# Kernel optimization log

Measured on AMD Instinct MI355X. Metric: run time of the kernel, lower is better.

The kernel has to match this reference:

```python
import jax, jax.numpy as jnp
import numpy as np

DIM = 1024
D_STATE = 16

def setup_inputs() -> dict:
    key = jax.random.key(0)
    kx, ka, kd = jax.random.split(key, 3)
    x = jax.random.normal(kx, (4, 8192, DIM), dtype=jnp.float32)
    A = jax.random.normal(ka, (DIM, D_STATE), dtype=jnp.float32)
    D = jax.random.normal(kd, (D_STATE, DIM), dtype=jnp.float32)
    return {"x": x, "A": A, "D": D}

def reference(x, A, D):
    # x: [B, N, C]; A: [C, S]; D: [S, C]
    x_state = jnp.einsum('bnc,cs->bns', x, A)        # [B, N, S]
    x_state = jnp.cumsum(x_state, axis=1)            # prefix sum over sequence
    out = jnp.einsum('bns,sc->bnc', x_state, D)      # [B, N, C]
    return out
```

## Files before the change

### kernel.cpp

```cpp
#include <hip/hip_runtime.h>

#define DIM   1024
#define DST   16
#define NSEQ  8192
#define NB    4

#define MT    64
#define KC    128
#define KCP   132
#define NTILE 128

__global__ __launch_bounds__(256) void kA_gemm_scan(
    const float* __restrict__ x, const float* __restrict__ A,
    float* __restrict__ Tloc, float* __restrict__ TS)
{
    __shared__ float xs[MT * KC];
    __shared__ float at[DST * KCP];
    __shared__ float scanbuf[16 * DST];

    const int t    = threadIdx.x;
    const int b    = blockIdx.x >> 7;
    const int tile = blockIdx.x & 127;
    const int n0   = tile * MT;

    const int kq4 = t >> 6;
    const int mg  = (t >> 2) & 15;
    const int sp  = t & 3;

    const float* xrow = x + ((long)(b * NSEQ + n0)) * DIM;

    float acc[4][4];
    #pragma unroll
    for (int r = 0; r < 4; ++r)
        #pragma unroll
        for (int j = 0; j < 4; ++j) acc[r][j] = 0.f;

    const int kbase = kq4 * 32;

    for (int kc = 0; kc < DIM; kc += KC) {
        {
            const int q  = t & 31;
            const int r0 = t >> 5;
            #pragma unroll
            for (int it = 0; it < 8; ++it) {
                const int m  = it * 8 + r0;
                const float4 v = *(const float4*)(xrow + (long)m * DIM + kc + 4 * q);
                const int qs = q ^ ((m >> 2) & 7);
                *(float4*)&xs[m * KC + 4 * qs] = v;
            }
        }
        {
            #pragma unroll
            for (int it = 0; it < 8; ++it) {
                const int idx = it * 256 + t;
                const int kl  = idx >> 4;
                const int ss  = idx & 15;
                at[ss * KCP + kl] = A[(kc + kl) * DST + ss];
            }
        }
        __syncthreads();

        #pragma unroll
        for (int kq = 0; kq < 8; ++kq) {
            const int kqi = (kbase >> 2) + kq;
            const float4 a0 = *(const float4*)&at[(sp +  0) * KCP + kbase + 4 * kq];
            const float4 a1 = *(const float4*)&at[(sp +  4) * KCP + kbase + 4 * kq];
            const float4 a2 = *(const float4*)&at[(sp +  8) * KCP + kbase + 4 * kq];
            const float4 a3 = *(const float4*)&at[(sp + 12) * KCP + kbase + 4 * kq];
            const int qs = kqi ^ (mg & 7);
            #pragma unroll
            for (int r = 0; r < 4; ++r) {
                const float4 xv = *(const float4*)&xs[(mg * 4 + r) * KC + 4 * qs];
                acc[r][0] += xv.x * a0.x + xv.y * a0.y + xv.z * a0.z + xv.w * a0.w;
                acc[r][1] += xv.x * a1.x + xv.y * a1.y + xv.z * a1.z + xv.w * a1.w;
                acc[r][2] += xv.x * a2.x + xv.y * a2.y + xv.z * a2.z + xv.w * a2.w;
                acc[r][3] += xv.x * a3.x + xv.y * a3.y + xv.z * a3.z + xv.w * a3.w;
            }
        }
        __syncthreads();
    }

    float* red = xs;
    #pragma unroll
    for (int r = 0; r < 4; ++r)
        #pragma unroll
        for (int j = 0; j < 4; ++j)
            red[kq4 * (64 * 17) + (mg * 4 + r) * 17 + (sp + 4 * j)] = acc[r][j];
    __syncthreads();

    const int s   = t & 15;
    const int mg2 = t >> 4;
    float acc0 = 0.f, acc1 = 0.f, acc2 = 0.f, acc3 = 0.f;
    #pragma unroll
    for (int q = 0; q < 4; ++q) {
        const float* rq = red + q * (64 * 17) + (mg2 * 4) * 17 + s;
        acc0 += rq[0 * 17];
        acc1 += rq[1 * 17];
        acc2 += rq[2 * 17];
        acc3 += rq[3 * 17];
    }
    __syncthreads();

    const float rsum = acc0 + acc1 + acc2 + acc3;
    scanbuf[mg2 * DST + s] = rsum;
    __syncthreads();
    float excl = 0.f, total = 0.f;
    #pragma unroll
    for (int m = 0; m < 16; ++m) {
        const float v = scanbuf[m * DST + s];
        total += v;
        excl  += (m < mg2) ? v : 0.f;
    }
    if (mg2 == 0) TS[((long)b * NTILE + tile) * DST + s] = total;

    const float c0 = excl + acc0;
    const float c1 = c0 + acc1;
    const float c2 = c1 + acc2;
    const float c3 = c2 + acc3;
    *(float4*)&Tloc[((long)(b * DST + s)) * NSEQ + n0 + mg2 * 4] =
        make_float4(c0, c1, c2, c3);
}

__global__ __launch_bounds__(256) void kB_scan_out(
    const float* __restrict__ Tloc, const float* __restrict__ TS,
    const float* __restrict__ D, float* __restrict__ out)
{
    __shared__ float sp[MT * 20];
    __shared__ float partial[16 * DST];
    __shared__ float basebuf[DST];

    const int t    = threadIdx.x;
    const int b    = blockIdx.x >> 7;
    const int tile = blockIdx.x & 127;
    const int n0   = tile * MT;
    const int s    = t & 15;
    const int mg   = t >> 4;

    float4 dreg[16];
    #pragma unroll
    for (int ss = 0; ss < 16; ++ss)
        dreg[ss] = *(const float4*)&D[ss * DIM + 4 * t];

    {
        const float* tsb = TS + (long)b * NTILE * DST;
        float p = 0.f;
        for (int j = mg; j < tile; j += 16) p += tsb[j * DST + s];
        partial[mg * DST + s] = p;
    }
    __syncthreads();
    {
        float bsum = 0.f;
        #pragma unroll
        for (int m = 0; m < 16; ++m) bsum += partial[m * DST + s];
        if (mg == 0) basebuf[s] = bsum;
    }
    __syncthreads();

    #pragma unroll
    for (int j = 0; j < 4; ++j) {
        const int idx = j * 256 + t;
        const int ss  = idx >> 6;
        const int nn  = idx & 63;
        sp[nn * 20 + ss] = Tloc[((long)(b * DST + ss)) * NSEQ + n0 + nn] + basebuf[ss];
    }
    __syncthreads();

    float* ob = out + ((long)(b * NSEQ + n0)) * DIM + 4 * t;
    for (int r = 0; r < MT; ++r) {
        const float4 s0 = *(const float4*)&sp[r * 20 + 0];
        const float4 s1 = *(const float4*)&sp[r * 20 + 4];
        const float4 s2 = *(const float4*)&sp[r * 20 + 8];
        const float4 s3 = *(const float4*)&sp[r * 20 + 12];
        const float sv[16] = {s0.x, s0.y, s0.z, s0.w, s1.x, s1.y, s1.z, s1.w,
                              s2.x, s2.y, s2.z, s2.w, s3.x, s3.y, s3.z, s3.w};
        float4 o = make_float4(0.f, 0.f, 0.f, 0.f);
        #pragma unroll
        for (int ss = 0; ss < 16; ++ss) {
            o.x += sv[ss] * dreg[ss].x;
            o.y += sv[ss] * dreg[ss].y;
            o.z += sv[ss] * dreg[ss].z;
            o.w += sv[ss] * dreg[ss].w;
        }
        *(float4*)(ob + (long)r * DIM) = o;
    }
}

extern "C" void kernel_launch(void* const* d_in, const int* in_sizes, int n_in,
                              void* d_out, int out_size, void* d_ws, size_t ws_size,
                              hipStream_t stream) {
    const float* x = (const float*)d_in[0];
    const float* A = (const float*)d_in[1];
    const float* D = (const float*)d_in[2];
    float* out  = (float*)d_out;
    float* Tloc = (float*)d_ws;
    float* TS   = Tloc + (long)NB * DST * NSEQ;

    kA_gemm_scan<<<dim3(NB * NTILE), dim3(256), 0, stream>>>(x, A, Tloc, TS);
    kB_scan_out <<<dim3(NB * NTILE), dim3(256), 0, stream>>>(Tloc, TS, D, out);
}
```

Baseline: 271.1 us.

## Double-buffer x/A chunks with register prefetch in projection kernel

Kernel A now splits the K dimension into 16 chunks of 64 and keeps two LDS buffers for the x tile and the transposed A. Global loads for the next chunk go into registers while the current chunk is computed, then get stored to the other buffer, so only one barrier is needed per chunk. The aim is to hide global-memory latency behind the FMA work. The cost is extra live registers for the prefetched values, which may lower occupancy.

```diff
diff --git a/kernel.cpp b/kernel.cpp
--- a/kernel.cpp
+++ b/kernel.cpp
@@ -6,16 +6,17 @@
 #define NB    4
 
 #define MT    64
-#define KC    128
-#define KCP   132
+#define KC2   64
+#define NCH   16
+#define ATP   68
 #define NTILE 128
 
 __global__ __launch_bounds__(256) void kA_gemm_scan(
     const float* __restrict__ x, const float* __restrict__ A,
     float* __restrict__ Tloc, float* __restrict__ TS)
 {
-    __shared__ float xs[MT * KC];
-    __shared__ float at[DST * KCP];
+    __shared__ float xs[2][MT * KC2];
+    __shared__ float at[2][DST * ATP];
     __shared__ float scanbuf[16 * DST];
 
     const int t    = threadIdx.x;
@@ -23,9 +24,11 @@
     const int tile = blockIdx.x & 127;
     const int n0   = tile * MT;
 
-    const int kq4 = t >> 6;
+    const int w   = t >> 6;
     const int mg  = (t >> 2) & 15;
     const int sp  = t & 3;
+    const int sq  = t & 15;
+    const int sm  = t >> 4;
 
     const float* xrow = x + ((long)(b * NSEQ + n0)) * DIM;
 
@@ -35,57 +38,66 @@
         #pragma unroll
         for (int j = 0; j < 4; ++j) acc[r][j] = 0.f;
 
-    const int kbase = kq4 * 32;
-
-    for (int kc = 0; kc < DIM; kc += KC) {
-        {
-            const int q  = t & 31;
-            const int r0 = t >> 5;
-            #pragma unroll
-            for (int it = 0; it < 8; ++it) {
-                const int m  = it * 8 + r0;
-                const float4 v = *(const float4*)(xrow + (long)m * DIM + kc + 4 * q);
-                const int qs = q ^ ((m >> 2) & 7);
-                *(float4*)&xs[m * KC + 4 * qs] = v;
-            }
-        }
-        {
-            #pragma unroll
-            for (int it = 0; it < 8; ++it) {
-                const int idx = it * 256 + t;
-                const int kl  = idx >> 4;
-                const int ss  = idx & 15;
-                at[ss * KCP + kl] = A[(kc + kl) * DST + ss];
-            }
-        }
+    float4 xr0, xr1, xr2, xr3;
+    float  ar0, ar1, ar2, ar3;
+
+#define LOADX(c) do { const int kc_ = (c) * KC2;                               \
+    xr0 = *(const float4*)(xrow + (long)(sm +  0) * DIM + kc_ + 4 * sq);       \
+    xr1 = *(const float4*)(xrow + (long)(sm + 16) * DIM + kc_ + 4 * sq);       \
+    xr2 = *(const float4*)(xrow + (long)(sm + 32) * DIM + kc_ + 4 * sq);       \
+    xr3 = *(const float4*)(xrow + (long)(sm + 48) * DIM + kc_ + 4 * sq);       \
+    ar0 = A[(kc_ + ((0 * 256 + t) >> 4)) * DST + (t & 15)];                    \
+    ar1 = A[(kc_ + ((1 * 256 + t) >> 4)) * DST + (t & 15)];                    \
+    ar2 = A[(kc_ + ((2 * 256 + t) >> 4)) * DST + (t & 15)];                    \
+    ar3 = A[(kc_ + ((3 * 256 + t) >> 4)) * DST + (t & 15)]; } while (0)
+
+#define STORE(bb) do {                                                         \
+    *(float4*)&xs[bb][(sm +  0) * KC2 + 4 * (sq ^ (((sm +  0) >> 2) & 7))] = xr0; \
+    *(float4*)&xs[bb][(sm + 16) * KC2 + 4 * (sq ^ (((sm + 16) >> 2) & 7))] = xr1; \
+    *(float4*)&xs[bb][(sm + 32) * KC2 + 4 * (sq ^ (((sm + 32) >> 2) & 7))] = xr2; \
+    *(float4*)&xs[bb][(sm + 48) * KC2 + 4 * (sq ^ (((sm + 48) >> 2) & 7))] = xr3; \
+    at[bb][(t & 15) * ATP + ((0 * 256 + t) >> 4)] = ar0;                       \
+    at[bb][(t & 15) * ATP + ((1 * 256 + t) >> 4)] = ar1;                       \
+    at[bb][(t & 15) * ATP + ((2 * 256 + t) >> 4)] = ar2;                       \
+    at[bb][(t & 15) * ATP + ((3 * 256 + t) >> 4)] = ar3; } while (0)
+
+#define COMPUTE(bb) do {                                                       \
+    _Pragma("unroll")                                                          \
+    for (int kq = 0; kq < 4; ++kq) {                                           \
+        const int kb = w * 16 + 4 * kq;                                        \
+        const float4 a0 = *(const float4*)&at[bb][(sp +  0) * ATP + kb];       \
+        const float4 a1 = *(const float4*)&at[bb][(sp +  4) * ATP + kb];       \
+        const float4 a2 = *(const float4*)&at[bb][(sp +  8) * ATP + kb];       \
+        const float4 a3 = *(const float4*)&at[bb][(sp + 12) * ATP + kb];       \
+        const int qs = 4 * ((w * 4 + kq) ^ (mg & 7));                          \
+        _Pragma("unroll")                                                      \
+        for (int r = 0; r < 4; ++r) {                                          \
+            const float4 xv = *(const float4*)&xs[bb][(mg * 4 + r) * KC2 + qs];\
+            acc[r][0] += xv.x * a0.x + xv.y * a0.y + xv.z * a0.z + xv.w * a0.w;\
+            acc[r][1] += xv.x * a1.x + xv.y * a1.y + xv.z * a1.z + xv.w * a1.w;\
+            acc[r][2] += xv.x * a2.x + xv.y * a2.y + xv.z * a2.z + xv.w * a2.w;\
+            acc[r][3] += xv.x * a3.x + xv.y * a3.y + xv.z * a3.z + xv.w * a3.w;\
+        }                                                                      \
+    } } while (0)
+
+    LOADX(0);
+    STORE(0);
+    __syncthreads();
+
+    for (int c = 0; c < NCH; ++c) {
+        const int cur = c & 1;
+        if (c + 1 < NCH) LOADX(c + 1);
+        COMPUTE(cur);
+        if (c + 1 < NCH) STORE(cur ^ 1);
         __syncthreads();
-
-        #pragma unroll
-        for (int kq = 0; kq < 8; ++kq) {
-            const int kqi = (kbase >> 2) + kq;
-            const float4 a0 = *(const float4*)&at[(sp +  0) * KCP + kbase + 4 * kq];
-            const float4 a1 = *(const float4*)&at[(sp +  4) * KCP + kbase + 4 * kq];
-            const float4 a2 = *(const float4*)&at[(sp +  8) * KCP + kbase + 4 * kq];
-            const float4 a3 = *(const float4*)&at[(sp + 12) * KCP + kbase + 4 * kq];
-            const int qs = kqi ^ (mg & 7);
-            #pragma unroll
-            for (int r = 0; r < 4; ++r) {
-                const float4 xv = *(const float4*)&xs[(mg * 4 + r) * KC + 4 * qs];
-                acc[r][0] += xv.x * a0.x + xv.y * a0.y + xv.z * a0.z + xv.w * a0.w;
-                acc[r][1] += xv.x * a1.x + xv.y * a1.y + xv.z * a1.z + xv.w * a1.w;
-                acc[r][2] += xv.x * a2.x + xv.y * a2.y + xv.z * a2.z + xv.w * a2.w;
-                acc[r][3] += xv.x * a3.x + xv.y * a3.y + xv.z * a3.z + xv.w * a3.w;
-            }
-        }
-        __syncthreads();
-    }
-
-    float* red = xs;
+    }
+
+    float* red = &xs[0][0];
     #pragma unroll
     for (int r = 0; r < 4; ++r)
         #pragma unroll
         for (int j = 0; j < 4; ++j)
-            red[kq4 * (64 * 17) + (mg * 4 + r) * 17 + (sp + 4 * j)] = acc[r][j];
+            red[w * (64 * 17) + (mg * 4 + r) * 17 + (sp + 4 * j)] = acc[r][j];
     __syncthreads();
 
     const int s   = t & 15;
@@ -119,6 +131,9 @@
     const float c3 = c2 + acc3;
     *(float4*)&Tloc[((long)(b * DST + s)) * NSEQ + n0 + mg2 * 4] =
         make_float4(c0, c1, c2, c3);
+#undef LOADX
+#undef STORE
+#undef COMPUTE
 }
 
 __global__ __launch_bounds__(256) void kB_scan_out(
```

Result: no change. 276.3 us (+1.9%).
